# Performance work log

Hardware: AMD Instinct MI355X
Metric: run time of the kernel (lower is better)

Reference implementation:

```python
import jax, jax.numpy as jnp
import numpy as np

C = 256
NUM_HEADS = 8
GROUPS = 8
EPS = 1e-5


def setup_inputs() -> dict:
    key = jax.random.key(0)
    ks = jax.random.split(key, 7)
    B, H, W = 2, 64, 64
    x = jax.random.normal(ks[0], (B, C, H, W), dtype=jnp.float32)
    gn_weight = jnp.ones((C,), dtype=jnp.float32)
    gn_bias = jnp.zeros((C,), dtype=jnp.float32)
    # 1x1 convs == per-pixel linear layers
    w_qkv = jax.random.normal(ks[1], (3 * C, C), dtype=jnp.float32) * (1.0 / np.sqrt(C))
    b_qkv = jax.random.normal(ks[2], (3 * C,), dtype=jnp.float32) * 0.01
    w_proj = jax.random.normal(ks[3], (C, C), dtype=jnp.float32) * (1.0 / np.sqrt(C))
    b_proj = jax.random.normal(ks[4], (C,), dtype=jnp.float32) * 0.01
    return {"x": x, "gn_weight": gn_weight, "gn_bias": gn_bias,
            "w_qkv": w_qkv, "b_qkv": b_qkv, "w_proj": w_proj, "b_proj": b_proj}


def reference(x, gn_weight, gn_bias, w_qkv, b_qkv, w_proj, b_proj):
    B, Cc, H, W = x.shape
    nh = NUM_HEADS
    hd = Cc // nh
    N = H * W
    scale = hd ** (-0.5)

    # GroupNorm(8, C): normalize over (C/G, H, W) per group, biased variance
    xg = x.reshape(B, GROUPS, Cc // GROUPS, H, W)
    mean = xg.mean(axis=(2, 3, 4), keepdims=True)
    var = xg.var(axis=(2, 3, 4), keepdims=True)
    hn = (xg - mean) * jax.lax.rsqrt(var + EPS)
    hn = hn.reshape(B, Cc, H, W) * gn_weight[None, :, None, None] + gn_bias[None, :, None, None]

    hf = hn.reshape(B, Cc, N)                       # [B, C, N]
    qkv = jnp.einsum('oc,bcn->bon', w_qkv, hf) + b_qkv[None, :, None]  # [B, 3C, N]
    qkv = qkv.reshape(B, 3, nh, hd, N)
    # q,k,v: [B, nh, N, hd]
    q = jnp.transpose(qkv[:, 0], (0, 1, 3, 2))
    k = jnp.transpose(qkv[:, 1], (0, 1, 3, 2))
    v = jnp.transpose(qkv[:, 2], (0, 1, 3, 2))

    attn = jnp.einsum('bhqd,bhkd->bhqk', q, k) * scale  # [B, nh, N, N]
    attn = jax.nn.softmax(attn, axis=-1)
    o = jnp.einsum('bhqk,bhkd->bhqd', attn, v)           # [B, nh, N, hd]
    o = jnp.transpose(o, (0, 1, 3, 2)).reshape(B, Cc, H, W)

    of = o.reshape(B, Cc, N)
    out = jnp.einsum('oc,bcn->bon', w_proj, of) + b_proj[None, :, None]
    return out.reshape(B, Cc, H, W)
```

## Files before the change

### kernel.cpp

```cpp
#include <hip/hip_runtime.h>


typedef _Float16 half8 __attribute__((ext_vector_type(8)));
typedef __fp16   fp16x2 __attribute__((ext_vector_type(2)));
typedef float    f32x4 __attribute__((ext_vector_type(4)));
typedef int      int2v __attribute__((ext_vector_type(2)));

__device__ __forceinline__ f32x4 mfma16(half8 a, half8 b, f32x4 c) {
  return __builtin_amdgcn_mfma_f32_16x16x32_f16(a, b, c, 0, 0, 0);
}

#if __has_builtin(__builtin_amdgcn_exp2f)
#define EXP2(x) __builtin_amdgcn_exp2f(x)
#else
#define EXP2(x) exp2f(x)
#endif

__device__ __forceinline__ unsigned short h_bits(_Float16 h) {
  return __builtin_bit_cast(unsigned short, h);
}
__device__ __forceinline__ int h2_bits(fp16x2 h) {
  return __builtin_bit_cast(int, h);
}

constexpr float CSCALE = (float)(1.4426950408889634 / 5.656854249492381);
constexpr float LOSC   = 2048.0f;
constexpr float ILOSC  = 1.0f / 2048.0f;

__global__ __launch_bounds__(256) void gn_stats(const float* __restrict__ x,
                                                float* __restrict__ stats) {
  const int bg = blockIdx.x, ch = blockIdx.y, tid = threadIdx.x;
  const float* p = x + (size_t)bg * 131072 + (size_t)ch * 4096;
  float s = 0.f, ss = 0.f;
#pragma unroll
  for (int j = 0; j < 4; ++j) {
    f32x4 v = *(const f32x4*)(p + j * 1024 + tid * 4);
#pragma unroll
    for (int k = 0; k < 4; ++k) { s += v[k]; ss += v[k] * v[k]; }
  }
#pragma unroll
  for (int m = 1; m <= 32; m <<= 1) { s += __shfl_xor(s, m); ss += __shfl_xor(ss, m); }
  __shared__ float red[8];
  const int wv = tid >> 6;
  if ((tid & 63) == 0) { red[wv * 2] = s; red[wv * 2 + 1] = ss; }
  __syncthreads();
  if (tid == 0) {
    float S = red[0] + red[2] + red[4] + red[6];
    float SS = red[1] + red[3] + red[5] + red[7];
    atomicAdd(&stats[bg * 2], S);
    atomicAdd(&stats[bg * 2 + 1], SS);
  }
}

__global__ __launch_bounds__(256) void gn_apply(const float* __restrict__ x,
                                                const float* __restrict__ gw,
                                                const float* __restrict__ gb,
                                                const float* __restrict__ stats,
                                                _Float16* __restrict__ hn_hi,
                                                _Float16* __restrict__ hn_lo) {
  __shared__ float tile[64 * 65];
  const int tid = threadIdx.x;
  const int a = tid & 15;
  const int row16 = tid >> 4;
  const int b = blockIdx.z, c0 = blockIdx.y * 64, n0 = blockIdx.x * 64;
#pragma unroll
  for (int m = 0; m < 4; ++m) {
    const int cl = row16 + 16 * m;
    const int c = c0 + cl;
    const int g = c >> 5;
    const float s = stats[(b * 8 + g) * 2];
    const float ss = stats[(b * 8 + g) * 2 + 1];
    const float mean = s * (1.f / 131072.f);
    const float var = ss * (1.f / 131072.f) - mean * mean;
    const float rstd = rsqrtf(var + 1e-5f);
    const float ga = gw[c] * rstd;
    const float be = gb[c] - mean * ga;
    f32x4 xv = *(const f32x4*)(x + ((size_t)(b * 256 + c)) * 4096 + n0 + a * 4);
#pragma unroll
    for (int j = 0; j < 4; ++j) tile[cl * 65 + a * 4 + j] = xv[j] * ga + be;
  }
  __syncthreads();
#pragma unroll
  for (int m = 0; m < 4; ++m) {
    const int nl = row16 + 16 * m;
    const int cb = a * 4;
    unsigned short hh[4], ll[4];
#pragma unroll
    for (int j = 0; j < 4; ++j) {
      float v = tile[(cb + j) * 65 + nl];
      _Float16 h = (_Float16)v;
      hh[j] = h_bits(h);
      ll[j] = h_bits((_Float16)((v - (float)h) * LOSC));
    }
    int2v uh, ul;
    uh[0] = hh[0] | (hh[1] << 16); uh[1] = hh[2] | (hh[3] << 16);
    ul[0] = ll[0] | (ll[1] << 16); ul[1] = ll[2] | (ll[3] << 16);
    size_t off = ((size_t)(b * 4096 + n0 + nl)) * 256 + c0 + cb;
    *(int2v*)(hn_hi + off) = uh;
    *(int2v*)(hn_lo + off) = ul;
  }
}

__global__ __launch_bounds__(256) void wsplit(const float* __restrict__ wq,
                                              const float* __restrict__ wp,
                                              _Float16* __restrict__ wqh,
                                              _Float16* __restrict__ wql,
                                              _Float16* __restrict__ wph,
                                              _Float16* __restrict__ wpl) {
  const int idx = blockIdx.x * 256 + threadIdx.x;
  if (idx < 196608) {
    float v = wq[idx];
    _Float16 h = (_Float16)v;
    wqh[idx] = h;
    wql[idx] = (_Float16)((v - (float)h) * LOSC);
  } else {
    const int i2 = idx - 196608;
    float v = wp[i2];
    _Float16 h = (_Float16)v;
    wph[i2] = h;
    wpl[i2] = (_Float16)((v - (float)h) * LOSC);
  }
}

template <int MODE>
__global__ __launch_bounds__(256) void gemm_split(
    const _Float16* __restrict__ Ahi, const _Float16* __restrict__ Alo,
    const _Float16* __restrict__ Bhi, const _Float16* __restrict__ Blo,
    const float* __restrict__ bias,
    _Float16* __restrict__ qkT, _Float16* __restrict__ v_t,
    float* __restrict__ outp) {
  __shared__ _Float16 a_lds[8192];
  __shared__ _Float16 b_lds[8192];
  const int tid = threadIdx.x, lane = tid & 63, wv = tid >> 6;
  const int qq = lane >> 4, ii = lane & 15;
  const int m0 = blockIdx.x * 64, n0 = blockIdx.y * 64, bz = blockIdx.z;
  const int hlT = (tid >> 7) & 1, cT = (tid >> 6) & 1;
  const int qT = (tid >> 4) & 3, iT = tid & 15;
  const _Float16* Asel = hlT ? Alo : Ahi;
  const _Float16* Bsel = hlT ? Blo : Bhi;
  const _Float16* aptr = Asel + (size_t)(m0 + iT) * 256 + 32 * cT + 8 * qT;
  const _Float16* bptr = Bsel + ((size_t)(bz * 4096 + n0 + iT)) * 256 + 32 * cT + 8 * qT;

  f32x4 acc[4] = {}, acc2[4] = {};
  for (int k0 = 0; k0 < 256; k0 += 64) {
#pragma unroll
    for (int j = 0; j < 4; ++j) {
      *(half8*)(a_lds + (((j * 2 + hlT) * 2 + cT) * 64 + (tid & 63)) * 8) =
          *(const half8*)(aptr + (size_t)(16 * j) * 256 + k0);
      *(half8*)(b_lds + (((j * 2 + hlT) * 2 + cT) * 64 + (tid & 63)) * 8) =
          *(const half8*)(bptr + (size_t)(16 * j) * 256 + k0);
    }
    __syncthreads();
    half8 ah[2], al[2];
#pragma unroll
    for (int c = 0; c < 2; ++c) {
      ah[c] = *(const half8*)(a_lds + (((wv * 2 + 0) * 2 + c) * 64 + lane) * 8);
      al[c] = *(const half8*)(a_lds + (((wv * 2 + 1) * 2 + c) * 64 + lane) * 8);
    }
#pragma unroll
    for (int t = 0; t < 4; ++t) {
#pragma unroll
      for (int c = 0; c < 2; ++c) {
        half8 bh_ = *(const half8*)(b_lds + (((t * 2 + 0) * 2 + c) * 64 + lane) * 8);
        half8 bl_ = *(const half8*)(b_lds + (((t * 2 + 1) * 2 + c) * 64 + lane) * 8);
        acc[t]  = mfma16(ah[c], bh_, acc[t]);
        acc2[t] = mfma16(ah[c], bl_, acc2[t]);
        acc2[t] = mfma16(al[c], bh_, acc2[t]);
      }
    }
    __syncthreads();
  }

  const int och0 = m0 + 16 * wv + 4 * qq;
  if (MODE == 0) {
    if (m0 < 512) {
      const float sc = (m0 < 256) ? CSCALE : 1.0f;
#pragma unroll
      for (int t = 0; t < 4; ++t) {
        const int n = n0 + 16 * t + ii;
        unsigned short hh[4];
#pragma unroll
        for (int r = 0; r < 4; ++r) {
          float val = (acc[t][r] + acc2[t][r] * ILOSC + bias[och0 + r]) * sc;
          hh[r] = h_bits((_Float16)val);
        }
        int2v u;
        u[0] = hh[0] | (hh[1] << 16);
        u[1] = hh[2] | (hh[3] << 16);
        *(int2v*)(qkT + ((size_t)(bz * 4096 + n)) * 512 + och0) = u;
      }
    } else {
#pragma unroll
      for (int t = 0; t < 4; ++t) {
#pragma unroll
        for (int r = 0; r < 4; ++r) {
          const int och = och0 + r;
          const int d = och - 512;
          const int hd_ = d & 31, head = d >> 5;
          const int n = n0 + 16 * t + ii;
          float val = acc[t][r] + acc2[t][r] * ILOSC + bias[och];
          v_t[((size_t)((bz * 8 + head) * 32 + hd_)) * 4096 + n] = (_Float16)val;
        }
      }
    }
  } else {
#pragma unroll
    for (int t = 0; t < 4; ++t) {
#pragma unroll
      for (int r = 0; r < 4; ++r) {
        const int och = och0 + r;
        const int n = n0 + 16 * t + ii;
        outp[((size_t)(bz * 256 + och)) * 4096 + n] =
            acc[t][r] + acc2[t][r] * ILOSC + bias[och];
      }
    }
  }
}

__global__ __launch_bounds__(512) void attn_kernel(
    const _Float16* __restrict__ qkT, const _Float16* __restrict__ v_t,
    _Float16* __restrict__ o_hi, _Float16* __restrict__ o_lo) {
  __shared__ _Float16 k_lds[2][2048];
  __shared__ _Float16 v_lds[2][2048];
  __shared__ _Float16 p_lds[10240];
  const int tid = threadIdx.x, lane = tid & 63, wv = tid >> 6;
  const int qq = lane >> 4, ii = lane & 15;
  const int bh = blockIdx.y, b = bh >> 3, h = bh & 7;
  const int n0 = blockIdx.x * 128;

  half8 qf = *(const half8*)(qkT + ((size_t)(b * 4096 + n0 + 16 * wv + ii)) * 512 +
                             h * 32 + 8 * qq);

  const int u = tid & 255;
  const int ch = u >> 6, qt = (u >> 4) & 3, it = u & 15;
  const bool isK = tid < 256;
  const _Float16* src =
      isK ? qkT + ((size_t)b * 4096) * 512 + 256 + h * 32 +
                (size_t)(4 * it + ch) * 512 + 8 * qt
          : v_t + ((size_t)(bh * 32 + it + 16 * (ch & 1))) * 4096 +
                32 * (ch >> 1) + 8 * qt;
  const size_t kstep = isK ? (size_t)64 * 512 : (size_t)64;
  _Float16* dstA = (isK ? k_lds[0] : v_lds[0]) + u * 8;
  _Float16* dstB = (isK ? k_lds[1] : v_lds[1]) + u * 8;

  half8 ones;
#pragma unroll
  for (int j = 0; j < 8; ++j) ones[j] = (_Float16)1.0f;

  f32x4 o0 = {}, o1 = {}, accl = {};

  half8 reg = *(const half8*)src;
  *(half8*)dstA = reg;
  __syncthreads();

  for (int kb = 0; kb < 64; ++kb) {
    const int cur = kb & 1;
    if (kb < 63) reg = *(const half8*)(src + (size_t)(kb + 1) * kstep);

    const _Float16* kbase = k_lds[cur];
    const _Float16* vbase = v_lds[cur];

    f32x4 s[4];
#pragma unroll
    for (int t = 0; t < 4; ++t) {
      half8 kf = *(const half8*)(kbase + (t * 64 + lane) * 8);
      f32x4 z = {};
      s[t] = mfma16(qf, kf, z);
    }
#pragma unroll
    for (int r = 0; r < 4; ++r) {
      float p0 = EXP2(s[0][r]), p1 = EXP2(s[1][r]);
      float p2 = EXP2(s[2][r]), p3 = EXP2(s[3][r]);
      int2v pu;
      pu[0] = h2_bits(__builtin_amdgcn_cvt_pkrtz(p0, p1));
      pu[1] = h2_bits(__builtin_amdgcn_cvt_pkrtz(p2, p3));
      *(int2v*)(p_lds + wv * 1280 + (qq * 4 + r) * 80 + 4 * ii) = pu;
    }
#pragma unroll
    for (int c = 0; c < 2; ++c) {
      half8 pf = *(const half8*)(p_lds + wv * 1280 + ii * 80 + 32 * c + 8 * qq);
      half8 vf0 = *(const half8*)(vbase + ((c * 2 + 0) * 64 + lane) * 8);
      half8 vf1 = *(const half8*)(vbase + ((c * 2 + 1) * 64 + lane) * 8);
      o0 = mfma16(pf, vf0, o0);
      o1 = mfma16(pf, vf1, o1);
      accl = mfma16(pf, ones, accl);
    }

    if (kb < 63) *(half8*)(cur ? dstA : dstB) = reg;
    __syncthreads();
  }

#pragma unroll
  for (int r = 0; r < 4; ++r) {
    const float inv = 1.0f / accl[r];
    const size_t row =
        ((size_t)(b * 4096 + n0 + 16 * wv + 4 * qq + r)) * 256 + h * 32 + ii;
    float v0 = o0[r] * inv, v1 = o1[r] * inv;
    _Float16 h0 = (_Float16)v0;
    o_hi[row] = h0;
    o_lo[row] = (_Float16)((v0 - (float)h0) * LOSC);
    _Float16 h1 = (_Float16)v1;
    o_hi[row + 16] = h1;
    o_lo[row + 16] = (_Float16)((v1 - (float)h1) * LOSC);
  }
}

extern "C" void kernel_launch(void* const* d_in, const int* in_sizes, int n_in,
                              void* d_out, int out_size, void* d_ws, size_t ws_size,
                              hipStream_t stream) {
  const float* x     = (const float*)d_in[0];
  const float* gnw   = (const float*)d_in[1];
  const float* gnb   = (const float*)d_in[2];
  const float* wqkv  = (const float*)d_in[3];
  const float* bqkv  = (const float*)d_in[4];
  const float* wproj = (const float*)d_in[5];
  const float* bproj = (const float*)d_in[6];
  float* out = (float*)d_out;

  char* ws = (char*)d_ws;
  size_t off = 0;
  auto alloc = [&](size_t bytes) -> char* {
    char* p = ws + off;
    off += (bytes + 255) & ~(size_t)255;
    return p;
  };
  float*    stats  = (float*)alloc(128);
  _Float16* hn_hi  = (_Float16*)alloc((size_t)2 * 4096 * 256 * 2);
  _Float16* hn_lo  = (_Float16*)alloc((size_t)2 * 4096 * 256 * 2);
  _Float16* wq_hi  = (_Float16*)alloc((size_t)768 * 256 * 2);
  _Float16* wq_lo  = (_Float16*)alloc((size_t)768 * 256 * 2);
  _Float16* wp_hi  = (_Float16*)alloc((size_t)256 * 256 * 2);
  _Float16* wp_lo  = (_Float16*)alloc((size_t)256 * 256 * 2);
  _Float16* qkT    = (_Float16*)alloc((size_t)2 * 4096 * 512 * 2);
  _Float16* v_t    = (_Float16*)alloc((size_t)16 * 32 * 4096 * 2);
  _Float16* o_hi   = (_Float16*)alloc((size_t)2 * 4096 * 256 * 2);
  _Float16* o_lo   = (_Float16*)alloc((size_t)2 * 4096 * 256 * 2);
  if (off > ws_size) return;

  (void)hipMemsetAsync(stats, 0, 256, stream);
  gn_stats<<<dim3(16, 32), 256, 0, stream>>>(x, stats);
  gn_apply<<<dim3(64, 4, 2), 256, 0, stream>>>(x, gnw, gnb, stats, hn_hi, hn_lo);
  wsplit<<<1024, 256, 0, stream>>>(wqkv, wproj, wq_hi, wq_lo, wp_hi, wp_lo);
  gemm_split<0><<<dim3(12, 64, 2), 256, 0, stream>>>(wq_hi, wq_lo, hn_hi, hn_lo,
                                                     bqkv, qkT, v_t, nullptr);
  attn_kernel<<<dim3(32, 16), 512, 0, stream>>>(qkT, v_t, o_hi, o_lo);
  gemm_split<1><<<dim3(4, 64, 2), 256, 0, stream>>>(wp_hi, wp_lo, o_hi, o_lo,
                                                    bproj, nullptr, nullptr, out);
}
```

Measured before the change: 177.1 us.

## Compute transposed scores so P stays in registers, dropping the P LDS round-trip

The attention kernel now computes S^T = K·Q^T, so each lane's exponentiated scores already sit in the B-operand layout of a 16x16x16 MFMA for the PV product. This removes the per-tile write and read of P through shared memory. Key/value tiles grow to 128 keys per iteration, stored in padded LDS layouts, which halves the loop trip count and the number of barriers. The output stores become packed 4-wide writes. In exchange the kernel uses the lower-K MFMA for PV and the row-sum, which means more MFMA instructions per key, and the padded LDS layout changes bank-access patterns.

```diff
diff --git a/kernel.cpp b/kernel.cpp
--- a/kernel.cpp
+++ b/kernel.cpp
@@ -2,12 +2,16 @@
 
 
 typedef _Float16 half8 __attribute__((ext_vector_type(8)));
+typedef _Float16 half4 __attribute__((ext_vector_type(4)));
 typedef __fp16   fp16x2 __attribute__((ext_vector_type(2)));
 typedef float    f32x4 __attribute__((ext_vector_type(4)));
 typedef int      int2v __attribute__((ext_vector_type(2)));
 
 __device__ __forceinline__ f32x4 mfma16(half8 a, half8 b, f32x4 c) {
   return __builtin_amdgcn_mfma_f32_16x16x32_f16(a, b, c, 0, 0, 0);
+}
+__device__ __forceinline__ f32x4 mfma16k16(half4 a, half4 b, f32x4 c) {
+  return __builtin_amdgcn_mfma_f32_16x16x16f16(a, b, c, 0, 0, 0);
 }
 
 #if __has_builtin(__builtin_amdgcn_exp2f)
@@ -220,9 +224,8 @@
 __global__ __launch_bounds__(512) void attn_kernel(
     const _Float16* __restrict__ qkT, const _Float16* __restrict__ v_t,
     _Float16* __restrict__ o_hi, _Float16* __restrict__ o_lo) {
-  __shared__ _Float16 k_lds[2][2048];
-  __shared__ _Float16 v_lds[2][2048];
-  __shared__ _Float16 p_lds[10240];
+  __shared__ _Float16 k_lds[2][128 * 40];
+  __shared__ _Float16 v_lds[2][32 * 136];
   const int tid = threadIdx.x, lane = tid & 63, wv = tid >> 6;
   const int qq = lane >> 4, ii = lane & 15;
   const int bh = blockIdx.y, b = bh >> 3, h = bh & 7;
@@ -231,78 +234,87 @@
   half8 qf = *(const half8*)(qkT + ((size_t)(b * 4096 + n0 + 16 * wv + ii)) * 512 +
                              h * 32 + 8 * qq);
 
-  const int u = tid & 255;
-  const int ch = u >> 6, qt = (u >> 4) & 3, it = u & 15;
-  const bool isK = tid < 256;
-  const _Float16* src =
-      isK ? qkT + ((size_t)b * 4096) * 512 + 256 + h * 32 +
-                (size_t)(4 * it + ch) * 512 + 8 * qt
-          : v_t + ((size_t)(bh * 32 + it + 16 * (ch & 1))) * 4096 +
-                32 * (ch >> 1) + 8 * qt;
-  const size_t kstep = isK ? (size_t)64 * 512 : (size_t)64;
-  _Float16* dstA = (isK ? k_lds[0] : v_lds[0]) + u * 8;
-  _Float16* dstB = (isK ? k_lds[1] : v_lds[1]) + u * 8;
-
-  half8 ones;
-#pragma unroll
-  for (int j = 0; j < 8; ++j) ones[j] = (_Float16)1.0f;
+  const int kkey = tid >> 2, kq = tid & 3;
+  const _Float16* ksrc = qkT + ((size_t)(b * 4096 + kkey)) * 512 + 256 + h * 32 + 8 * kq;
+  const int kdst = kkey * 40 + 8 * kq;
+  const int vd = tid >> 4, vc = tid & 15;
+  const _Float16* vsrc = v_t + ((size_t)(bh * 32 + vd)) * 4096 + 8 * vc;
+  const int vdst = vd * 136 + 8 * vc;
+
+  half4 onesf;
+#pragma unroll
+  for (int j = 0; j < 4; ++j) onesf[j] = (_Float16)1.0f;
 
   f32x4 o0 = {}, o1 = {}, accl = {};
 
-  half8 reg = *(const half8*)src;
-  *(half8*)dstA = reg;
+  half8 kreg = *(const half8*)ksrc;
+  half8 vreg = *(const half8*)vsrc;
+  *(half8*)(k_lds[0] + kdst) = kreg;
+  *(half8*)(v_lds[0] + vdst) = vreg;
   __syncthreads();
 
-  for (int kb = 0; kb < 64; ++kb) {
+  for (int kb = 0; kb < 32; ++kb) {
     const int cur = kb & 1;
-    if (kb < 63) reg = *(const half8*)(src + (size_t)(kb + 1) * kstep);
-
+    if (kb < 31) {
+      kreg = *(const half8*)(ksrc + (size_t)(kb + 1) * 128 * 512);
+      vreg = *(const half8*)(vsrc + (size_t)(kb + 1) * 128);
+    }
     const _Float16* kbase = k_lds[cur];
     const _Float16* vbase = v_lds[cur];
 
-    f32x4 s[4];
-#pragma unroll
-    for (int t = 0; t < 4; ++t) {
-      half8 kf = *(const half8*)(kbase + (t * 64 + lane) * 8);
+#pragma unroll
+    for (int t = 0; t < 8; ++t) {
+      half8 kf = *(const half8*)(kbase + (16 * t + ii) * 40 + 8 * qq);
       f32x4 z = {};
-      s[t] = mfma16(qf, kf, z);
-    }
-#pragma unroll
-    for (int r = 0; r < 4; ++r) {
-      float p0 = EXP2(s[0][r]), p1 = EXP2(s[1][r]);
-      float p2 = EXP2(s[2][r]), p3 = EXP2(s[3][r]);
-      int2v pu;
-      pu[0] = h2_bits(__builtin_amdgcn_cvt_pkrtz(p0, p1));
-      pu[1] = h2_bits(__builtin_amdgcn_cvt_pkrtz(p2, p3));
-      *(int2v*)(p_lds + wv * 1280 + (qq * 4 + r) * 80 + 4 * ii) = pu;
-    }
-#pragma unroll
-    for (int c = 0; c < 2; ++c) {
-      half8 pf = *(const half8*)(p_lds + wv * 1280 + ii * 80 + 32 * c + 8 * qq);
-      half8 vf0 = *(const half8*)(vbase + ((c * 2 + 0) * 64 + lane) * 8);
-      half8 vf1 = *(const half8*)(vbase + ((c * 2 + 1) * 64 + lane) * 8);
-      o0 = mfma16(pf, vf0, o0);
-      o1 = mfma16(pf, vf1, o1);
-      accl = mfma16(pf, ones, accl);
-    }
-
-    if (kb < 63) *(half8*)(cur ? dstA : dstB) = reg;
+      f32x4 st = mfma16(kf, qf, z);
+      fp16x2 e01 = __builtin_amdgcn_cvt_pkrtz(EXP2(st[0]), EXP2(st[1]));
+      fp16x2 e23 = __builtin_amdgcn_cvt_pkrtz(EXP2(st[2]), EXP2(st[3]));
+      int2v pi;
+      pi[0] = h2_bits(e01);
+      pi[1] = h2_bits(e23);
+      half4 pt = __builtin_bit_cast(half4, pi);
+      half4 vf0 = *(const half4*)(vbase + ii * 136 + 16 * t + 4 * qq);
+      half4 vf1 = *(const half4*)(vbase + (16 + ii) * 136 + 16 * t + 4 * qq);
+      o0 = mfma16k16(vf0, pt, o0);
+      o1 = mfma16k16(vf1, pt, o1);
+      accl = mfma16k16(onesf, pt, accl);
+    }
+
+    if (kb < 31) {
+      _Float16* knext = k_lds[cur ^ 1];
+      _Float16* vnext = v_lds[cur ^ 1];
+      *(half8*)(knext + kdst) = kreg;
+      *(half8*)(vnext + vdst) = vreg;
+    }
     __syncthreads();
   }
 
+  const float inv = 1.0f / accl[0];
+  const size_t row = ((size_t)(b * 4096 + n0 + 16 * wv + ii)) * 256 + h * 32;
+  unsigned short hh[4], ll[4];
 #pragma unroll
   for (int r = 0; r < 4; ++r) {
-    const float inv = 1.0f / accl[r];
-    const size_t row =
-        ((size_t)(b * 4096 + n0 + 16 * wv + 4 * qq + r)) * 256 + h * 32 + ii;
-    float v0 = o0[r] * inv, v1 = o1[r] * inv;
-    _Float16 h0 = (_Float16)v0;
-    o_hi[row] = h0;
-    o_lo[row] = (_Float16)((v0 - (float)h0) * LOSC);
-    _Float16 h1 = (_Float16)v1;
-    o_hi[row + 16] = h1;
-    o_lo[row + 16] = (_Float16)((v1 - (float)h1) * LOSC);
-  }
+    float v = o0[r] * inv;
+    _Float16 hv = (_Float16)v;
+    hh[r] = h_bits(hv);
+    ll[r] = h_bits((_Float16)((v - (float)hv) * LOSC));
+  }
+  int2v uh, ul;
+  uh[0] = hh[0] | (hh[1] << 16); uh[1] = hh[2] | (hh[3] << 16);
+  ul[0] = ll[0] | (ll[1] << 16); ul[1] = ll[2] | (ll[3] << 16);
+  *(int2v*)(o_hi + row + 4 * qq) = uh;
+  *(int2v*)(o_lo + row + 4 * qq) = ul;
+#pragma unroll
+  for (int r = 0; r < 4; ++r) {
+    float v = o1[r] * inv;
+    _Float16 hv = (_Float16)v;
+    hh[r] = h_bits(hv);
+    ll[r] = h_bits((_Float16)((v - (float)hv) * LOSC));
+  }
+  uh[0] = hh[0] | (hh[1] << 16); uh[1] = hh[2] | (hh[3] << 16);
+  ul[0] = ll[0] | (ll[1] << 16); ul[1] = ll[2] | (ll[3] << 16);
+  *(int2v*)(o_hi + row + 16 + 4 * qq) = uh;
+  *(int2v*)(o_lo + row + 16 + 4 * qq) = ul;
 }
 
 extern "C" void kernel_launch(void* const* d_in, const int* in_sizes, int n_in,
```

After: 182.4 us. +3.0%, slower.
